# Kernel optimization log

Hardware: AMD Instinct MI355X
Metric: run time of the kernel (lower is better)

Reference implementation:

```python
import jax, jax.numpy as jnp
import numpy as np

LAMBD = 0.5  # config.training.loss.lambd


def setup_inputs() -> dict:
    key = jax.random.key(0)
    ka, kb = jax.random.split(key)
    a = jax.random.normal(ka, (16384, 512), dtype=jnp.float32)
    b = jax.random.normal(kb, (16384, 512), dtype=jnp.float32)
    return {"a": a, "b": b}


def reference(a, b):
    # loss = 2 * lambd * sum(a @ b.T)
    # Mathematically identical (up to fp reassociation) to
    # 2 * lambd * dot(colsum(a), colsum(b)), avoiding the [N, M] intermediate.
    loss = 2.0 * LAMBD * jnp.dot(jnp.sum(a, axis=0), jnp.sum(b, axis=0))
    return loss
```

## Files before the change

kernel.cpp:

```cpp
#include <hip/hip_runtime.h>


#define ROWS  16384
#define COLS  512
#define NBLK1 1024
#define NTHR1 256
#define N4    ((ROWS * COLS) / 4)
#define NT1   (NBLK1 * NTHR1)


__global__ __launch_bounds__(NTHR1) void colsum_partial(
        const float4* __restrict__ a, const float4* __restrict__ b,
        float4* __restrict__ pa, float4* __restrict__ pb) {
    const int tid = threadIdx.x;
    const int g0  = blockIdx.x * NTHR1 + tid;

    float4 sa = make_float4(0.f, 0.f, 0.f, 0.f);
    float4 sb = make_float4(0.f, 0.f, 0.f, 0.f);

#pragma unroll
    for (int i = 0; i < 8; ++i) {
        float4 x = a[g0 + i * NT1];
        sa.x += x.x; sa.y += x.y; sa.z += x.z; sa.w += x.w;
    }
#pragma unroll
    for (int i = 0; i < 8; ++i) {
        float4 y = b[g0 + i * NT1];
        sb.x += y.x; sb.y += y.y; sb.z += y.z; sb.w += y.w;
    }

    __shared__ float4 la[128];
    __shared__ float4 lb[128];
    if (tid >= 128) {
        la[tid - 128] = sa;
        lb[tid - 128] = sb;
    }
    __syncthreads();
    if (tid < 128) {
        float4 oa = la[tid];
        float4 ob = lb[tid];
        sa.x += oa.x; sa.y += oa.y; sa.z += oa.z; sa.w += oa.w;
        sb.x += ob.x; sb.y += ob.y; sb.z += ob.z; sb.w += ob.w;
        pa[blockIdx.x * 128 + tid] = sa;
        pb[blockIdx.x * 128 + tid] = sb;
    }
}

__global__ __launch_bounds__(64) void reduce_dot(
        const float* __restrict__ pa, const float* __restrict__ pb,
        float* __restrict__ out) {
    const int l   = threadIdx.x;
    const int col = blockIdx.x * 16 + (l & 15);
    const int r0  = l >> 4;

    float va = 0.f, vb = 0.f;
#pragma unroll 8
    for (int r = r0; r < NBLK1; r += 4) {
        va += pa[r * COLS + col];
        vb += pb[r * COLS + col];
    }
    va += __shfl_xor(va, 16, 64); va += __shfl_xor(va, 32, 64);
    vb += __shfl_xor(vb, 16, 64); vb += __shfl_xor(vb, 32, 64);
    float p = va * vb;
    p += __shfl_xor(p, 1, 64);
    p += __shfl_xor(p, 2, 64);
    p += __shfl_xor(p, 4, 64);
    p += __shfl_xor(p, 8, 64);
    if (l == 0) {
        atomicAdd(out, p);
    }
}

extern "C" void kernel_launch(void* const* d_in, const int* in_sizes, int n_in,
                              void* d_out, int out_size, void* d_ws, size_t ws_size,
                              hipStream_t stream) {
    const float4* a = (const float4*)d_in[0];
    const float4* b = (const float4*)d_in[1];
    float* out = (float*)d_out;

    float4* pa = (float4*)d_ws;
    float4* pb = pa + NBLK1 * (COLS / 4);

    hipMemsetAsync(out, 0, sizeof(float), stream);

    colsum_partial<<<NBLK1, NTHR1, 0, stream>>>(a, b, pa, pb);

    reduce_dot<<<COLS / 16, 64, 0, stream>>>((const float*)pa, (const float*)pb, out);
}
```

Baseline: 108.8 us.

## Drop memset, use nontemporal loads, halve partial blocks, widen final reduction

Removes the separate hipMemsetAsync by zeroing the output inside the first kernel. The column-sum kernel now runs half as many blocks, each doing 16 interleaved nontemporal vector loads of a and b instead of 8 sequential ones per array. The second kernel uses 256 threads with a shared-memory combine to reduce the smaller partial buffer. Zeroing out inside kernel 1 relies on stream ordering before kernel 2's atomics, and fewer blocks may reduce the latency hiding available for the bandwidth-bound reads.

```diff
diff --git a/kernel.cpp b/kernel.cpp
--- a/kernel.cpp
+++ b/kernel.cpp
@@ -3,87 +3,96 @@
 
 #define ROWS  16384
 #define COLS  512
-#define NBLK1 1024
-#define NTHR1 256
+#define PB    512
+#define NTHR  256
 #define N4    ((ROWS * COLS) / 4)
-#define NT1   (NBLK1 * NTHR1)
+#define NT    (PB * NTHR)
+
+typedef float vfloat4 __attribute__((ext_vector_type(4)));
+
+__device__ __forceinline__ vfloat4 ntload(const vfloat4* p) {
+    return __builtin_nontemporal_load(p);
+}
 
 
-__global__ __launch_bounds__(NTHR1) void colsum_partial(
-        const float4* __restrict__ a, const float4* __restrict__ b,
-        float4* __restrict__ pa, float4* __restrict__ pb) {
+__global__ __launch_bounds__(NTHR) void colsum_partial(
+        const vfloat4* __restrict__ a, const vfloat4* __restrict__ b,
+        vfloat4* __restrict__ pa, vfloat4* __restrict__ pb,
+        float* __restrict__ out) {
     const int tid = threadIdx.x;
-    const int g0  = blockIdx.x * NTHR1 + tid;
+    const int g0  = blockIdx.x * NTHR + tid;
 
-    float4 sa = make_float4(0.f, 0.f, 0.f, 0.f);
-    float4 sb = make_float4(0.f, 0.f, 0.f, 0.f);
+    if (blockIdx.x == 0 && tid == 0) out[0] = 0.0f;
+
+    vfloat4 sa = (vfloat4)(0.f);
+    vfloat4 sb = (vfloat4)(0.f);
 
 #pragma unroll
-    for (int i = 0; i < 8; ++i) {
-        float4 x = a[g0 + i * NT1];
-        sa.x += x.x; sa.y += x.y; sa.z += x.z; sa.w += x.w;
-    }
-#pragma unroll
-    for (int i = 0; i < 8; ++i) {
-        float4 y = b[g0 + i * NT1];
-        sb.x += y.x; sb.y += y.y; sb.z += y.z; sb.w += y.w;
+    for (int i = 0; i < 16; ++i) {
+        vfloat4 x = ntload(a + g0 + i * NT);
+        vfloat4 y = ntload(b + g0 + i * NT);
+        sa += x;
+        sb += y;
     }
 
-    __shared__ float4 la[128];
-    __shared__ float4 lb[128];
+    __shared__ vfloat4 la[128];
+    __shared__ vfloat4 lb[128];
     if (tid >= 128) {
         la[tid - 128] = sa;
         lb[tid - 128] = sb;
     }
     __syncthreads();
     if (tid < 128) {
-        float4 oa = la[tid];
-        float4 ob = lb[tid];
-        sa.x += oa.x; sa.y += oa.y; sa.z += oa.z; sa.w += oa.w;
-        sb.x += ob.x; sb.y += ob.y; sb.z += ob.z; sb.w += ob.w;
+        sa += la[tid];
+        sb += lb[tid];
         pa[blockIdx.x * 128 + tid] = sa;
         pb[blockIdx.x * 128 + tid] = sb;
     }
 }
 
-__global__ __launch_bounds__(64) void reduce_dot(
+__global__ __launch_bounds__(NTHR) void reduce_dot(
         const float* __restrict__ pa, const float* __restrict__ pb,
         float* __restrict__ out) {
-    const int l   = threadIdx.x;
-    const int col = blockIdx.x * 16 + (l & 15);
-    const int r0  = l >> 4;
+    const int t   = threadIdx.x;
+    const int col = blockIdx.x * 16 + (t & 15);
+    const int rc  = t >> 4;
 
     float va = 0.f, vb = 0.f;
 #pragma unroll 8
-    for (int r = r0; r < NBLK1; r += 4) {
+    for (int r = rc; r < PB; r += 16) {
         va += pa[r * COLS + col];
         vb += pb[r * COLS + col];
     }
     va += __shfl_xor(va, 16, 64); va += __shfl_xor(va, 32, 64);
     vb += __shfl_xor(vb, 16, 64); vb += __shfl_xor(vb, 32, 64);
-    float p = va * vb;
-    p += __shfl_xor(p, 1, 64);
-    p += __shfl_xor(p, 2, 64);
-    p += __shfl_xor(p, 4, 64);
-    p += __shfl_xor(p, 8, 64);
-    if (l == 0) {
-        atomicAdd(out, p);
+
+    __shared__ float sa4[4][16];
+    __shared__ float sb4[4][16];
+    const int wave = t >> 6, lane = t & 63;
+    if (lane < 16) { sa4[wave][lane] = va; sb4[wave][lane] = vb; }
+    __syncthreads();
+    if (t < 16) {
+        float ca = sa4[0][t] + sa4[1][t] + sa4[2][t] + sa4[3][t];
+        float cb = sb4[0][t] + sb4[1][t] + sb4[2][t] + sb4[3][t];
+        float p  = ca * cb;
+        p += __shfl_xor(p, 1, 64);
+        p += __shfl_xor(p, 2, 64);
+        p += __shfl_xor(p, 4, 64);
+        p += __shfl_xor(p, 8, 64);
+        if (t == 0) atomicAdd(out, p);
     }
 }
 
 extern "C" void kernel_launch(void* const* d_in, const int* in_sizes, int n_in,
                               void* d_out, int out_size, void* d_ws, size_t ws_size,
                               hipStream_t stream) {
-    const float4* a = (const float4*)d_in[0];
-    const float4* b = (const float4*)d_in[1];
+    const vfloat4* a = (const vfloat4*)d_in[0];
+    const vfloat4* b = (const vfloat4*)d_in[1];
     float* out = (float*)d_out;
 
-    float4* pa = (float4*)d_ws;
-    float4* pb = pa + NBLK1 * (COLS / 4);
+    vfloat4* pa = (vfloat4*)d_ws;
+    vfloat4* pb = pa + PB * (COLS / 4);
 
-    hipMemsetAsync(out, 0, sizeof(float), stream);
-
-    colsum_partial<<<NBLK1, NTHR1, 0, stream>>>(a, b, pa, pb);
-
-    reduce_dot<<<COLS / 16, 64, 0, stream>>>((const float*)pa, (const float*)pb, out);
+    colsum_partial<<<PB, NTHR, 0, stream>>>(a, b, pa, pb, out);
+    reduce_dot<<<COLS / 16, NTHR, 0, stream>>>((const float*)pa, (const float*)pb, out);
 }
```

New measurement: 100.5 us. -7.6%, faster.
